# Performance work log

Hardware: AMD Instinct MI355X
Metric: run time of the kernel (lower is better)

The kernel has to match this reference:

```python
import jax, jax.numpy as jnp
import numpy as np

NEG_INF = float(np.finfo(np.float32).min)
B, QLEN, MLEN, KLEN = 2, 1024, 1024, 1024
KDIM = QDIM = ADIM = 1024
H = 16
DK = ADIM // H
SCALE = float(np.sqrt(DK))


def setup_inputs() -> dict:
    root = jax.random.key(0)
    ks = jax.random.split(root, 20)
    s = 0.02  # weight init std to keep logits well-scaled
    return {
        "key": jax.random.normal(ks[0], (B, KLEN, KDIM), jnp.float32),
        "query": jax.random.normal(ks[1], (B, QLEN, QDIM), jnp.float32),
        "memory": jax.random.normal(ks[2], (B, MLEN, KDIM), jnp.float32),
        "pos_embs": jax.random.normal(ks[3], (MLEN + KLEN, 1, QDIM), jnp.float32),
        "mask": jax.random.randint(ks[4], (B, QLEN, MLEN + KLEN), 0, 2, jnp.int32),
        "u": jax.random.normal(ks[5], (H, DK), jnp.float32) * s,
        "v": jax.random.normal(ks[6], (H, DK), jnp.float32) * s,
        "Wk": jax.random.normal(ks[7], (ADIM, KDIM), jnp.float32) * s,
        "bk": jnp.zeros((ADIM,), jnp.float32),
        "Wv": jax.random.normal(ks[8], (ADIM, KDIM), jnp.float32) * s,
        "bv": jnp.zeros((ADIM,), jnp.float32),
        "Wq": jax.random.normal(ks[9], (ADIM, QDIM), jnp.float32) * s,
        "bq": jnp.zeros((ADIM,), jnp.float32),
        "Wp": jax.random.normal(ks[10], (ADIM, QDIM), jnp.float32) * s,
        "bp": jnp.zeros((ADIM,), jnp.float32),
        "Wo": jax.random.normal(ks[11], (KDIM, ADIM), jnp.float32) * s,
        "bo": jnp.zeros((KDIM,), jnp.float32),
    }


def rel_shift(xs):
    # xs: [B, qlen, klen, H] -> TransformerXL pad/reshape shift trick
    b, q, k, h = xs.shape
    x = jnp.transpose(xs, (1, 2, 0, 3)).reshape(q, k, b * h)
    x = jnp.concatenate([jnp.zeros((q, 1, b * h), xs.dtype), x], axis=1)
    x = x.reshape(k + 1, q, b * h)[1:].reshape(q, k, b * h)
    return jnp.transpose(x.reshape(q, k, b, h), (2, 0, 1, 3))


def reference(key, query, memory, pos_embs, mask, u, v,
              Wk, bk, Wv, bv, Wq, bq, Wp, bp, Wo, bo):
    bs, qlen = query.shape[:2]
    kcat = jnp.concatenate([memory, key], axis=1)  # [B, mlen+klen, kdim]
    tk = kcat.shape[1]
    value = (kcat @ Wv.T + bv).reshape(bs, tk, H, DK)
    k = (kcat @ Wk.T + bk).reshape(bs, tk, H, DK)
    q = (query @ Wq.T + bq).reshape(bs, qlen, H, DK)
    p = (pos_embs.reshape(-1, pos_embs.shape[-1]) @ Wp.T + bp).reshape(-1, H, DK)
    AC = jnp.einsum('bihd,bjhd->bijh', q + u[None, None], k)
    BD = jnp.einsum('bihd,jhd->bijh', q + v[None, None], p)
    BD = rel_shift(BD)
    e = (AC + BD) / SCALE  # [B, qlen, mlen+klen, H]
    e = jnp.where(mask[..., None] == 0, NEG_INF, e)
    aw = jax.nn.softmax(e, axis=2)
    cv = jnp.einsum('bijh,bjhd->bihd', aw, value).reshape(bs, qlen, H * DK)
    cv = cv @ Wo.T + bo
    return cv, jnp.transpose(aw, (0, 3, 1, 2))
```

## Files before the change

kernel.cpp:

```cpp
#include <hip/hip_runtime.h>

using bf16x8 = __attribute__((ext_vector_type(8))) short;
using bf16x4 = __attribute__((ext_vector_type(4))) short;
using f32x4  = __attribute__((ext_vector_type(4))) float;

#define NH    16
#define DKH   64
#define TTOT  2048
#define QL    1024

__device__ __forceinline__ float bf2f(unsigned short u) {
  union { unsigned int i; float f; } c; c.i = ((unsigned int)u) << 16; return c.f;
}
__device__ __forceinline__ unsigned short f2bf(float f) {
  union { float f; unsigned int i; } c; c.f = f;
  unsigned int x = c.i;
  x += 0x7fffu + ((x >> 16) & 1u);
  return (unsigned short)(x >> 16);
}
__device__ __forceinline__ unsigned int cvtpk(float lo, float hi) {
  unsigned int r;
  asm("v_cvt_pk_bf16_f32 %0, %1, %2" : "=v"(r) : "v"(lo), "v"(hi));
  return r;
}
__device__ __forceinline__ int swz(int r, int c) {
  return r * 2048 + ((((c << 1) ^ ((r & 7) << 4))) >> 1);
}
__device__ __forceinline__ f32x4 mfma16(bf16x8 a, bf16x8 b, f32x4 c) {
  return __builtin_amdgcn_mfma_f32_16x16x32_bf16(a, b, c, 0, 0, 0);
}

__global__ void convert_all(
    const float* __restrict__ key, const float* __restrict__ query,
    const float* __restrict__ memory, const float* __restrict__ pos,
    const int* __restrict__ mask,
    const float* __restrict__ Wk, const float* __restrict__ Wv,
    const float* __restrict__ Wq, const float* __restrict__ Wp,
    const float* __restrict__ Wo,
    unsigned short* __restrict__ kcat, unsigned short* __restrict__ qbf,
    unsigned short* __restrict__ posb,
    unsigned short* __restrict__ wkb, unsigned short* __restrict__ wvb,
    unsigned short* __restrict__ wqb, unsigned short* __restrict__ wpb,
    unsigned short* __restrict__ wob, unsigned short* __restrict__ mkb)
{
  const int g0 = 1048576;
  const int g1 = g0 + 524288;
  const int g2 = g1 + 524288;
  const int g3 = g2 + 262144;
  const int g4 = g3 + 262144;
  const int g5 = g4 + 262144;
  const int g6 = g5 + 262144;
  const int g7 = g6 + 262144;
  const int g8 = g7 + 1048576;
  for (int g = blockIdx.x * blockDim.x + threadIdx.x; g < g8;
       g += gridDim.x * blockDim.x) {
    const float* src = nullptr;
    unsigned short* dst = nullptr;
    int i;
    if (g < g0) {
      i = g * 4;
      int b = i >> 21, r = i & ((1 << 21) - 1);
      int t = r >> 10, c = r & 1023;
      src = (t < 1024) ? memory + ((size_t)b << 20) + (t << 10) + c
                       : key + ((size_t)b << 20) + ((t - 1024) << 10) + c;
      dst = kcat + i;
    } else if (g < g1) { i = (g - g0) * 4; src = query + i; dst = qbf + i; }
    else if (g < g2)   { i = (g - g1) * 4; src = pos + i;   dst = posb + i; }
    else if (g < g3)   { i = (g - g2) * 4; src = Wk + i;    dst = wkb + i; }
    else if (g < g4)   { i = (g - g3) * 4; src = Wv + i;    dst = wvb + i; }
    else if (g < g5)   { i = (g - g4) * 4; src = Wq + i;    dst = wqb + i; }
    else if (g < g6)   { i = (g - g5) * 4; src = Wp + i;    dst = wpb + i; }
    else if (g < g7)   { i = (g - g6) * 4; src = Wo + i;    dst = wob + i; }
    else {
      i = (g - g7) * 4;
      const int4 mv = *(const int4*)(mask + i);
      const unsigned int nm = f2bf(-1e30f);
      uint2 o;
      o.x = (mv.x ? 0u : nm) | ((mv.y ? 0u : nm) << 16);
      o.y = (mv.z ? 0u : nm) | ((mv.w ? 0u : nm) << 16);
      *(uint2*)(mkb + i) = o;
      continue;
    }
    const float4 v = *(const float4*)src;
    uint2 o;
    o.x = cvtpk(v.x, v.y);
    o.y = cvtpk(v.z, v.w);
    *(uint2*)dst = o;
  }
}

#define GEMM_CORE(Aptr, Bptr) \
  f32x4 acc[4][4] = {}; \
  { \
    bf16x8 ra0 = *(const bf16x8*)Ap0; \
    bf16x8 ra1 = *(const bf16x8*)Ap1; \
    bf16x8 rb0 = *(const bf16x8*)Bp0; \
    bf16x8 rb1 = *(const bf16x8*)Bp1; \
    for (int kt = 0; kt < 32; ++kt) { \
      *(bf16x8*)(sA + swA0) = ra0; \
      *(bf16x8*)(sA + swA1) = ra1; \
      *(bf16x8*)(sB + swA0) = rb0; \
      *(bf16x8*)(sB + swA1) = rb1; \
      __syncthreads(); \
      if (kt + 1 < 32) { \
        const int o = (kt + 1) * 32; \
        ra0 = *(const bf16x8*)(Ap0 + o); \
        ra1 = *(const bf16x8*)(Ap1 + o); \
        rb0 = *(const bf16x8*)(Bp0 + o); \
        rb1 = *(const bf16x8*)(Bp1 + o); \
      } \
      bf16x8 af[4], bfr[4]; \
      _Pragma("unroll") \
      for (int mi = 0; mi < 4; ++mi) { \
        int row = wm + mi * 16 + l15; \
        af[mi] = *(const bf16x8*)(sA + row * 32 + ((l4 ^ ((row >> 1) & 3)) * 8)); \
      } \
      _Pragma("unroll") \
      for (int ni = 0; ni < 4; ++ni) { \
        int row = wn + ni * 16 + l15; \
        bfr[ni] = *(const bf16x8*)(sB + row * 32 + ((l4 ^ ((row >> 1) & 3)) * 8)); \
      } \
      _Pragma("unroll") \
      for (int mi = 0; mi < 4; ++mi) \
        _Pragma("unroll") \
        for (int ni = 0; ni < 4; ++ni) \
          acc[mi][ni] = mfma16(af[mi], bfr[ni], acc[mi][ni]); \
      __syncthreads(); \
    } \
  }

#define GEMM_PREAMBLE(Asrc, Bsrc) \
  constexpr int K = 1024; \
  __shared__ unsigned short sA[128 * 32]; \
  __shared__ unsigned short sB[128 * 32]; \
  const int tid = threadIdx.x; \
  const int lane = tid & 63; \
  const int wid = tid >> 6; \
  const int wm = (wid >> 1) * 64, wn = (wid & 1) * 64; \
  const int bm = blockIdx.y * 128, bn = blockIdx.x * 128; \
  const int l15 = lane & 15, l4 = lane >> 4; \
  const int c0 = tid, c1 = tid + 256; \
  const int am0 = c0 >> 2, as0 = c0 & 3; \
  const int am1 = c1 >> 2, as1 = c1 & 3; \
  const unsigned short* Ap0 = Asrc + (size_t)(bm + am0) * K + as0 * 8; \
  const unsigned short* Ap1 = Asrc + (size_t)(bm + am1) * K + as1 * 8; \
  const unsigned short* Bp0 = Bsrc + (size_t)(bn + am0) * K + as0 * 8; \
  const unsigned short* Bp1 = Bsrc + (size_t)(bn + am1) * K + as1 * 8; \
  const int swA0 = am0 * 32 + ((as0 ^ ((am0 >> 1) & 3)) * 8); \
  const int swA1 = am1 * 32 + ((as1 ^ ((am1 >> 1) & 3)) * 8);

__global__ __launch_bounds__(256, 2) void gemm_kv(
    const unsigned short* __restrict__ A, const unsigned short* __restrict__ Bw,
    const float* __restrict__ bk, const float* __restrict__ bv,
    unsigned short* __restrict__ kpk, unsigned short* __restrict__ vpk)
{
  GEMM_PREAMBLE(A, Bw)
  GEMM_CORE(A, Bw)
  const bool isK = bn < 1024;
  #pragma unroll
  for (int mi = 0; mi < 4; ++mi) {
    #pragma unroll
    for (int ni = 0; ni < 4; ++ni) {
      const int col = bn + wn + ni * 16 + l15;
      const int cc = col & 1023;
      const float bval = isK ? bk[cc] : bv[cc];
      #pragma unroll
      for (int j = 0; j < 4; ++j) {
        const int row = bm + wm + mi * 16 + l4 * 4 + j;
        const float cv = acc[mi][ni][j] + bval;
        const int bI = row >> 11;
        const int t = row & 2047;
        const int bh2 = bI * NH + (cc >> 6);
        if (isK) {
          const size_t o = ((((size_t)bh2 * 128 + (t >> 4)) * 8 +
                            ((cc & 63) >> 3)) * 16 + (t & 15)) * 8 + (cc & 7);
          kpk[o] = f2bf(cv);
        } else {
          const int dk = cc & 63;
          const size_t o = (((((size_t)bh2 * 4 + (dk >> 4)) * 64 + (t >> 5)) * 4 +
                            ((t >> 3) & 3)) * 16 + (dk & 15)) * 8 + (t & 7);
          vpk[o] = f2bf(cv);
        }
      }
    }
  }
}

__global__ __launch_bounds__(256, 2) void gemm_qp(
    const unsigned short* __restrict__ qry, const unsigned short* __restrict__ posb,
    const unsigned short* __restrict__ wqb, const unsigned short* __restrict__ wpb,
    const float* __restrict__ bq, const float* __restrict__ bp,
    const float* __restrict__ uvec, const float* __restrict__ vvec,
    unsigned short* __restrict__ qupk, unsigned short* __restrict__ qvpk,
    unsigned short* __restrict__ ppk)
{
  const bool isQ = blockIdx.z == 0;
  const unsigned short* A  = isQ ? qry : posb;
  const unsigned short* Bw = isQ ? wqb : wpb;
  GEMM_PREAMBLE(A, Bw)
  GEMM_CORE(A, Bw)
  #pragma unroll
  for (int mi = 0; mi < 4; ++mi) {
    #pragma unroll
    for (int ni = 0; ni < 4; ++ni) {
      const int col = bn + wn + ni * 16 + l15;
      #pragma unroll
      for (int j = 0; j < 4; ++j) {
        const int row = bm + wm + mi * 16 + l4 * 4 + j;
        if (isQ) {
          const float cv = acc[mi][ni][j] + bq[col];
          const int bI = row >> 10;
          const int t = row & 1023;
          const int bh2 = bI * NH + (col >> 6);
          const size_t o = ((((size_t)bh2 * 64 + (t >> 4)) * 8 +
                            ((col & 63) >> 3)) * 16 + (t & 15)) * 8 + (col & 7);
          qupk[o] = f2bf(cv + uvec[col]);
          qvpk[o] = f2bf(cv + vvec[col]);
        } else {
          const float cv = acc[mi][ni][j] + bp[col];
          const int t = row;
          const int h2 = col >> 6;
          const size_t o = ((((size_t)h2 * 128 + (t >> 4)) * 8 +
                            ((col & 63) >> 3)) * 16 + (t & 15)) * 8 + (col & 7);
          ppk[o] = f2bf(cv);
        }
      }
    }
  }
}

__global__ __launch_bounds__(256, 2) void gemm_out(
    const unsigned short* __restrict__ A, const unsigned short* __restrict__ Bw,
    const float* __restrict__ bias, float* __restrict__ outf)
{
  GEMM_PREAMBLE(A, Bw)
  GEMM_CORE(A, Bw)
  #pragma unroll
  for (int mi = 0; mi < 4; ++mi) {
    #pragma unroll
    for (int ni = 0; ni < 4; ++ni) {
      const int col = bn + wn + ni * 16 + l15;
      const float bval = bias[col];
      #pragma unroll
      for (int j = 0; j < 4; ++j) {
        const int row = bm + wm + mi * 16 + l4 * 4 + j;
        outf[(size_t)row * 1024 + col] = acc[mi][ni][j] + bval;
      }
    }
  }
}

__global__ __launch_bounds__(1024, 8) void attn_fused(
    const unsigned short* __restrict__ qupk, const unsigned short* __restrict__ qvpk,
    const unsigned short* __restrict__ kpk, const unsigned short* __restrict__ ppk,
    const unsigned short* __restrict__ vpk, const unsigned short* __restrict__ mkb,
    float* __restrict__ awout, unsigned short* __restrict__ cvb)
{
  __shared__ unsigned short sbd[16 * 2048];
  __shared__ float sred0[16][16];
  __shared__ float spv[3][4][16][16];
  const int tid = threadIdx.x;
  const int lane = tid & 63;
  const int w = tid >> 6;
  const int l15 = lane & 15, l4 = lane >> 4;

  const int wg = blockIdx.x;
  const int xcd = wg & 7, idx = wg >> 3;
  const int bh = xcd * 4 + (idx & 3);
  const int tI = idx >> 2;
  const int I0 = tI * 16;
  const int b = bh >> 4, h = bh & 15;

  {
    const unsigned short* qvt = qvpk + ((size_t)bh * 64 + tI) * 1024;
    bf16x8 a0 = *(const bf16x8*)(qvt + l4 * 128 + l15 * 8);
    bf16x8 a1 = *(const bf16x8*)(qvt + (4 + l4) * 128 + l15 * 8);
    const unsigned short* ppk_h = ppk + (size_t)h * 131072;
    #pragma unroll 2
    for (int nj = 0; nj < 8; ++nj) {
      const int tile = w * 8 + nj;
      const unsigned short* pt = ppk_h + (size_t)tile * 1024;
      bf16x8 b0 = *(const bf16x8*)(pt + l4 * 128 + l15 * 8);
      bf16x8 b1 = *(const bf16x8*)(pt + (4 + l4) * 128 + l15 * 8);
      f32x4 c = {0.f, 0.f, 0.f, 0.f};
      c = mfma16(a0, b0, c);
      c = mfma16(a1, b1, c);
      const int jj = tile * 16 + l15;
      #pragma unroll
      for (int j = 0; j < 4; ++j) {
        const int rl = l4 * 4 + j;
        const int r = I0 + rl;
        int dst, jp;
        if (jj >= 1023 - r) { dst = rl;     jp = jj + r - 1023; }
        else                { dst = rl - 1; jp = jj + r + 1025; }
        if (dst >= 0) sbd[swz(dst, jp)] = f2bf(c[j]);
      }
    }
    if (I0 <= 1006 && w < 8) {
      const unsigned short* qvt2 = qvpk + ((size_t)bh * 64 + tI + 1) * 1024;
      bf16x8 a0e = *(const bf16x8*)(qvt2 + l4 * 128 + l15 * 8);
      bf16x8 a1e = *(const bf16x8*)(qvt2 + (4 + l4) * 128 + l15 * 8);
      #pragma unroll 2
      for (int nj = 0; nj < 8; ++nj) {
        const int tile = w * 8 + nj;
        const unsigned short* pt = ppk_h + (size_t)tile * 1024;
        bf16x8 b0 = *(const bf16x8*)(pt + l4 * 128 + l15 * 8);
        bf16x8 b1 = *(const bf16x8*)(pt + (4 + l4) * 128 + l15 * 8);
        f32x4 c = {0.f, 0.f, 0.f, 0.f};
        c = mfma16(a0e, b0, c);
        c = mfma16(a1e, b1, c);
        const int jj = tile * 16 + l15;
        if (l4 == 0 && jj <= 1006 - I0)
          sbd[swz(15, jj + I0 + 1041)] = f2bf(c[0]);
      }
    }
    if (tid < 16) {
      const int jp = I0 + tid + 1025;
      if (jp < 2048) sbd[swz(tid, jp)] = 0;
    }
  }
  __syncthreads();

  {
    const unsigned short* qut = qupk + ((size_t)bh * 64 + tI) * 1024;
    bf16x8 a0 = *(const bf16x8*)(qut + l4 * 128 + l15 * 8);
    bf16x8 a1 = *(const bf16x8*)(qut + (4 + l4) * 128 + l15 * 8);
    const unsigned short* kpk_b = kpk + (size_t)bh * 131072;
    const unsigned short* mrow = mkb + ((size_t)b * QL + I0 + l15) * TTOT;
    const int rowbyte = l15 * 4096;
    const int sws = (l15 & 7) << 4;
    float sm = 0.f;
    #pragma unroll 2
    for (int nj = 0; nj < 8; ++nj) {
      const int tile = w * 8 + nj;
      const unsigned short* kt = kpk_b + (size_t)tile * 1024;
      bf16x8 b0 = *(const bf16x8*)(kt + l4 * 128 + l15 * 8);
      bf16x8 b1 = *(const bf16x8*)(kt + (4 + l4) * 128 + l15 * 8);
      f32x4 c = {0.f, 0.f, 0.f, 0.f};
      c = mfma16(b0, a0, c);
      c = mfma16(b1, a1, c);
      const int jp0 = tile * 16 + l4 * 4;
      char* sp = (char*)sbd + rowbyte + ((jp0 * 2) ^ sws);
      const bf16x4 bd4 = *(const bf16x4*)sp;
      const bf16x4 m4 = *(const bf16x4*)(mrow + jp0);
      bf16x4 pw;
      #pragma unroll
      for (int j = 0; j < 4; ++j) {
        const float s = (c[j] + bf2f((unsigned short)bd4[j])) * 0.125f +
                        bf2f((unsigned short)m4[j]);
        const float p = __expf(s);
        sm += p;
        pw[j] = (short)f2bf(p);
      }
      *(bf16x4*)sp = pw;
    }
    sm += __shfl_xor(sm, 16, 64);
    sm += __shfl_xor(sm, 32, 64);
    if (l4 == 0) sred0[w][l15] = sm;
  }
  __syncthreads();

  {
    const int r = w;
    float den = sred0[0][r];
    #pragma unroll
    for (int ww = 1; ww < 16; ++ww) den += sred0[ww][r];
    const float rinv = 1.0f / den;
    float* awb = awout + ((size_t)bh * QL + I0 + r) * TTOT;
    const int sws = (r & 7) << 4;
    #pragma unroll 2
    for (int q = 0; q < 4; ++q) {
      const int X = q * 1024 + lane * 16;
      bf16x8 vv = *(const bf16x8*)((const char*)sbd + r * 4096 + (X ^ sws));
      f32x4 lo, hi;
      #pragma unroll
      for (int k = 0; k < 4; ++k) {
        lo[k] = bf2f((unsigned short)vv[k]) * rinv;
        hi[k] = bf2f((unsigned short)vv[k + 4]) * rinv;
      }
      float* dp = awb + (X >> 1);
      *(f32x4*)dp = lo;
      *(f32x4*)(dp + 4) = hi;
    }
  }

  {
    const int dc = w & 3, kh = w >> 2;
    const unsigned short* vb = vpk + ((size_t)(bh * 4 + dc) * 64) * 512;
    const int sws = (l15 & 7) << 4;
    const int rowbyte = l15 * 4096;
    f32x4 pv = {0.f, 0.f, 0.f, 0.f};
    #pragma unroll 2
    for (int ks = kh * 16; ks < kh * 16 + 16; ++ks) {
      bf16x8 a = *(const bf16x8*)((const char*)sbd +
                  (rowbyte + ((ks * 64 + l4 * 16) ^ sws)));
      bf16x8 vvf = *(const bf16x8*)(vb + ks * 512 + lane * 8);
      pv = mfma16(a, vvf, pv);
    }
    if (kh) {
      #pragma unroll
      for (int j = 0; j < 4; ++j) spv[kh - 1][dc][l4 * 4 + j][l15] = pv[j];
    }
    __syncthreads();
    if (!kh) {
      const size_t obase = ((size_t)b * QL + I0 + l4 * 4) * 1024 + h * 64 + dc * 16 + l15;
      #pragma unroll
      for (int j = 0; j < 4; ++j) {
        const int rl = l4 * 4 + j;
        float den = sred0[0][rl];
        #pragma unroll
        for (int ww = 1; ww < 16; ++ww) den += sred0[ww][rl];
        const float o = (pv[j] + spv[0][dc][rl][l15] + spv[1][dc][rl][l15] +
                         spv[2][dc][rl][l15]) / den;
        cvb[obase + (size_t)j * 1024] = f2bf(o);
      }
    }
  }
}

extern "C" void kernel_launch(void* const* d_in, const int* in_sizes, int n_in,
                              void* d_out, int out_size, void* d_ws, size_t ws_size,
                              hipStream_t stream) {
  (void)in_sizes; (void)n_in; (void)out_size; (void)ws_size;
  const float* key    = (const float*)d_in[0];
  const float* query  = (const float*)d_in[1];
  const float* memory = (const float*)d_in[2];
  const float* pos    = (const float*)d_in[3];
  const int*   mask   = (const int*)d_in[4];
  const float* u      = (const float*)d_in[5];
  const float* v      = (const float*)d_in[6];
  const float* Wk     = (const float*)d_in[7];
  const float* bk     = (const float*)d_in[8];
  const float* Wv     = (const float*)d_in[9];
  const float* bv     = (const float*)d_in[10];
  const float* Wq     = (const float*)d_in[11];
  const float* bq     = (const float*)d_in[12];
  const float* Wp     = (const float*)d_in[13];
  const float* bp     = (const float*)d_in[14];
  const float* Wo     = (const float*)d_in[15];
  const float* bo     = (const float*)d_in[16];

  float* outCV = (float*)d_out;
  float* outAW = outCV + 2097152;

  char* ws = (char*)d_ws;
  const size_t MB = (size_t)1 << 20;
  unsigned short* kpk  = (unsigned short*)(ws + 0);
  unsigned short* vpk  = (unsigned short*)(ws + 8 * MB);
  unsigned short* qupk = (unsigned short*)(ws + 16 * MB);
  unsigned short* qvpk = (unsigned short*)(ws + 20 * MB);
  unsigned short* ppk  = (unsigned short*)(ws + 24 * MB);
  unsigned short* cvb  = (unsigned short*)(ws + 28 * MB);
  unsigned short* kcat = (unsigned short*)(ws + 32 * MB);
  unsigned short* qry  = (unsigned short*)(ws + 40 * MB);
  unsigned short* posb = (unsigned short*)(ws + 44 * MB);
  unsigned short* wkb  = (unsigned short*)(ws + 48 * MB);
  unsigned short* wvb  = (unsigned short*)(ws + 50 * MB);
  unsigned short* wqb  = (unsigned short*)(ws + 52 * MB);
  unsigned short* wpb  = (unsigned short*)(ws + 54 * MB);
  unsigned short* wob  = (unsigned short*)(ws + 56 * MB);
  unsigned short* mkb  = (unsigned short*)(ws + 58 * MB);

  convert_all<<<2048, 256, 0, stream>>>(key, query, memory, pos, mask,
      Wk, Wv, Wq, Wp, Wo, kcat, qry, posb, wkb, wvb, wqb, wpb, wob, mkb);

  gemm_kv<<<dim3(16, 32), 256, 0, stream>>>(kcat, wkb, bk, bv, kpk, vpk);
  gemm_qp<<<dim3(8, 16, 2), 256, 0, stream>>>(qry, posb, wqb, wpb, bq, bp,
      u, v, qupk, qvpk, ppk);

  attn_fused<<<2048, 1024, 0, stream>>>(qupk, qvpk, kpk, ppk, vpk, mkb,
      outAW, cvb);

  gemm_out<<<dim3(8, 16), 256, 0, stream>>>(cvb, wob, bo, outCV);
}
```

Baseline: 256.5 us.

## Merge projection GEMMs into one launch, truncate bf16 conversions, spread BD edge work

Combines the K/V and Q/P projection GEMMs into a single 768-block launch that picks its mode from the block index. This removes one kernel launch and lets the two groups of tiles run concurrently instead of back to back. Round-to-nearest bf16 conversion of BD values and softmax probabilities is replaced with plain truncation of the top 16 bits, which cuts ALU work but adds a small rounding bias. The extra BD row computation now uses all 16 waves with 4 tiles each instead of 8 waves with 8 tiles.

```diff
diff --git a/kernel.cpp b/kernel.cpp
--- a/kernel.cpp
+++ b/kernel.cpp
@@ -17,6 +17,9 @@
   unsigned int x = c.i;
   x += 0x7fffu + ((x >> 16) & 1u);
   return (unsigned short)(x >> 16);
+}
+__device__ __forceinline__ unsigned int fbits(float f) {
+  union { float f; unsigned int i; } c; c.f = f; return c.i;
 }
 __device__ __forceinline__ unsigned int cvtpk(float lo, float hi) {
   unsigned int r;
@@ -89,7 +92,7 @@
   }
 }
 
-#define GEMM_CORE(Aptr, Bptr) \
+#define GEMM_CORE() \
   f32x4 acc[4][4] = {}; \
   { \
     bf16x8 ra0 = *(const bf16x8*)Ap0; \
@@ -129,85 +132,72 @@
     } \
   }
 
-#define GEMM_PREAMBLE(Asrc, Bsrc) \
-  constexpr int K = 1024; \
+#define GEMM_PTRS(Asrc, Bsrc) \
+  const unsigned short* Ap0 = Asrc + (size_t)(bm + am0) * 1024 + as0 * 8; \
+  const unsigned short* Ap1 = Asrc + (size_t)(bm + am1) * 1024 + as1 * 8; \
+  const unsigned short* Bp0 = Bsrc + (size_t)(bn + am0) * 1024 + as0 * 8; \
+  const unsigned short* Bp1 = Bsrc + (size_t)(bn + am1) * 1024 + as1 * 8;
+
+#define GEMM_IDX() \
   __shared__ unsigned short sA[128 * 32]; \
   __shared__ unsigned short sB[128 * 32]; \
   const int tid = threadIdx.x; \
   const int lane = tid & 63; \
   const int wid = tid >> 6; \
   const int wm = (wid >> 1) * 64, wn = (wid & 1) * 64; \
-  const int bm = blockIdx.y * 128, bn = blockIdx.x * 128; \
   const int l15 = lane & 15, l4 = lane >> 4; \
-  const int c0 = tid, c1 = tid + 256; \
-  const int am0 = c0 >> 2, as0 = c0 & 3; \
-  const int am1 = c1 >> 2, as1 = c1 & 3; \
-  const unsigned short* Ap0 = Asrc + (size_t)(bm + am0) * K + as0 * 8; \
-  const unsigned short* Ap1 = Asrc + (size_t)(bm + am1) * K + as1 * 8; \
-  const unsigned short* Bp0 = Bsrc + (size_t)(bn + am0) * K + as0 * 8; \
-  const unsigned short* Bp1 = Bsrc + (size_t)(bn + am1) * K + as1 * 8; \
+  const int am0 = tid >> 2, as0 = tid & 3; \
+  const int am1 = (tid + 256) >> 2, as1 = (tid + 256) & 3; \
   const int swA0 = am0 * 32 + ((as0 ^ ((am0 >> 1) & 3)) * 8); \
   const int swA1 = am1 * 32 + ((as1 ^ ((am1 >> 1) & 3)) * 8);
 
-__global__ __launch_bounds__(256, 2) void gemm_kv(
-    const unsigned short* __restrict__ A, const unsigned short* __restrict__ Bw,
+__global__ __launch_bounds__(256, 2) void gemm_proj(
+    const unsigned short* __restrict__ kcat, const unsigned short* __restrict__ qry,
+    const unsigned short* __restrict__ posb,
+    const unsigned short* __restrict__ wkv, const unsigned short* __restrict__ wqb,
+    const unsigned short* __restrict__ wpb,
     const float* __restrict__ bk, const float* __restrict__ bv,
-    unsigned short* __restrict__ kpk, unsigned short* __restrict__ vpk)
+    const float* __restrict__ bq, const float* __restrict__ bp,
+    const float* __restrict__ uvec, const float* __restrict__ vvec,
+    unsigned short* __restrict__ kpk, unsigned short* __restrict__ vpk,
+    unsigned short* __restrict__ qupk, unsigned short* __restrict__ qvpk,
+    unsigned short* __restrict__ ppk)
 {
-  GEMM_PREAMBLE(A, Bw)
-  GEMM_CORE(A, Bw)
-  const bool isK = bn < 1024;
+  GEMM_IDX()
+  const int id = blockIdx.x;
+  int bm, bn, mode;
+  const unsigned short *A, *Bw;
+  if (id < 512)      { A = kcat; Bw = wkv; bm = (id >> 4) * 128; bn = (id & 15) * 128; mode = 0; }
+  else if (id < 640) { const int t = id - 512; A = qry;  Bw = wqb; bm = (t >> 3) * 128; bn = (t & 7) * 128; mode = 1; }
+  else               { const int t = id - 640; A = posb; Bw = wpb; bm = (t >> 3) * 128; bn = (t & 7) * 128; mode = 2; }
+  GEMM_PTRS(A, Bw)
+  GEMM_CORE()
   #pragma unroll
   for (int mi = 0; mi < 4; ++mi) {
     #pragma unroll
     for (int ni = 0; ni < 4; ++ni) {
       const int col = bn + wn + ni * 16 + l15;
-      const int cc = col & 1023;
-      const float bval = isK ? bk[cc] : bv[cc];
       #pragma unroll
       for (int j = 0; j < 4; ++j) {
         const int row = bm + wm + mi * 16 + l4 * 4 + j;
-        const float cv = acc[mi][ni][j] + bval;
-        const int bI = row >> 11;
-        const int t = row & 2047;
-        const int bh2 = bI * NH + (cc >> 6);
-        if (isK) {
-          const size_t o = ((((size_t)bh2 * 128 + (t >> 4)) * 8 +
-                            ((cc & 63) >> 3)) * 16 + (t & 15)) * 8 + (cc & 7);
-          kpk[o] = f2bf(cv);
-        } else {
-          const int dk = cc & 63;
-          const size_t o = (((((size_t)bh2 * 4 + (dk >> 4)) * 64 + (t >> 5)) * 4 +
-                            ((t >> 3) & 3)) * 16 + (dk & 15)) * 8 + (t & 7);
-          vpk[o] = f2bf(cv);
-        }
-      }
-    }
-  }
-}
-
-__global__ __launch_bounds__(256, 2) void gemm_qp(
-    const unsigned short* __restrict__ qry, const unsigned short* __restrict__ posb,
-    const unsigned short* __restrict__ wqb, const unsigned short* __restrict__ wpb,
-    const float* __restrict__ bq, const float* __restrict__ bp,
-    const float* __restrict__ uvec, const float* __restrict__ vvec,
-    unsigned short* __restrict__ qupk, unsigned short* __restrict__ qvpk,
-    unsigned short* __restrict__ ppk)
-{
-  const bool isQ = blockIdx.z == 0;
-  const unsigned short* A  = isQ ? qry : posb;
-  const unsigned short* Bw = isQ ? wqb : wpb;
-  GEMM_PREAMBLE(A, Bw)
-  GEMM_CORE(A, Bw)
-  #pragma unroll
-  for (int mi = 0; mi < 4; ++mi) {
-    #pragma unroll
-    for (int ni = 0; ni < 4; ++ni) {
-      const int col = bn + wn + ni * 16 + l15;
-      #pragma unroll
-      for (int j = 0; j < 4; ++j) {
-        const int row = bm + wm + mi * 16 + l4 * 4 + j;
-        if (isQ) {
+        if (mode == 0) {
+          const bool isK = col < 1024;
+          const int cc = col & 1023;
+          const float cv = acc[mi][ni][j] + (isK ? bk[cc] : bv[cc]);
+          const int bI = row >> 11;
+          const int t = row & 2047;
+          const int bh2 = bI * NH + (cc >> 6);
+          if (isK) {
+            const size_t o = ((((size_t)bh2 * 128 + (t >> 4)) * 8 +
+                              ((cc & 63) >> 3)) * 16 + (t & 15)) * 8 + (cc & 7);
+            kpk[o] = f2bf(cv);
+          } else {
+            const int dk = cc & 63;
+            const size_t o = (((((size_t)bh2 * 4 + (dk >> 4)) * 64 + (t >> 5)) * 4 +
+                              ((t >> 3) & 3)) * 16 + (dk & 15)) * 8 + (t & 7);
+            vpk[o] = f2bf(cv);
+          }
+        } else if (mode == 1) {
           const float cv = acc[mi][ni][j] + bq[col];
           const int bI = row >> 10;
           const int t = row & 1023;
@@ -233,8 +223,10 @@
     const unsigned short* __restrict__ A, const unsigned short* __restrict__ Bw,
     const float* __restrict__ bias, float* __restrict__ outf)
 {
-  GEMM_PREAMBLE(A, Bw)
-  GEMM_CORE(A, Bw)
+  GEMM_IDX()
+  const int bm = blockIdx.y * 128, bn = blockIdx.x * 128;
+  GEMM_PTRS(A, Bw)
+  GEMM_CORE()
   #pragma unroll
   for (int mi = 0; mi < 4; ++mi) {
     #pragma unroll
@@ -293,16 +285,16 @@
         int dst, jp;
         if (jj >= 1023 - r) { dst = rl;     jp = jj + r - 1023; }
         else                { dst = rl - 1; jp = jj + r + 1025; }
-        if (dst >= 0) sbd[swz(dst, jp)] = f2bf(c[j]);
-      }
-    }
-    if (I0 <= 1006 && w < 8) {
+        if (dst >= 0) sbd[swz(dst, jp)] = (unsigned short)(fbits(c[j]) >> 16);
+      }
+    }
+    if (I0 <= 1006) {
       const unsigned short* qvt2 = qvpk + ((size_t)bh * 64 + tI + 1) * 1024;
       bf16x8 a0e = *(const bf16x8*)(qvt2 + l4 * 128 + l15 * 8);
       bf16x8 a1e = *(const bf16x8*)(qvt2 + (4 + l4) * 128 + l15 * 8);
       #pragma unroll 2
-      for (int nj = 0; nj < 8; ++nj) {
-        const int tile = w * 8 + nj;
+      for (int nj = 0; nj < 4; ++nj) {
+        const int tile = w * 4 + nj;
         const unsigned short* pt = ppk_h + (size_t)tile * 1024;
         bf16x8 b0 = *(const bf16x8*)(pt + l4 * 128 + l15 * 8);
         bf16x8 b1 = *(const bf16x8*)(pt + (4 + l4) * 128 + l15 * 8);
@@ -311,7 +303,7 @@
         c = mfma16(a1e, b1, c);
         const int jj = tile * 16 + l15;
         if (l4 == 0 && jj <= 1006 - I0)
-          sbd[swz(15, jj + I0 + 1041)] = f2bf(c[0]);
+          sbd[swz(15, jj + I0 + 1041)] = (unsigned short)(fbits(c[0]) >> 16);
       }
     }
     if (tid < 16) {
@@ -343,16 +335,18 @@
       char* sp = (char*)sbd + rowbyte + ((jp0 * 2) ^ sws);
       const bf16x4 bd4 = *(const bf16x4*)sp;
       const bf16x4 m4 = *(const bf16x4*)(mrow + jp0);
-      bf16x4 pw;
+      float p[4];
       #pragma unroll
       for (int j = 0; j < 4; ++j) {
         const float s = (c[j] + bf2f((unsigned short)bd4[j])) * 0.125f +
                         bf2f((unsigned short)m4[j]);
-        const float p = __expf(s);
-        sm += p;
-        pw[j] = (short)f2bf(p);
-      }
-      *(bf16x4*)sp = pw;
+        p[j] = __expf(s);
+        sm += p[j];
+      }
+      uint2 pw;
+      pw.x = (fbits(p[1]) & 0xffff0000u) | (fbits(p[0]) >> 16);
+      pw.y = (fbits(p[3]) & 0xffff0000u) | (fbits(p[2]) >> 16);
+      *(uint2*)sp = pw;
     }
     sm += __shfl_xor(sm, 16, 64);
     sm += __shfl_xor(sm, 32, 64);
@@ -464,9 +458,8 @@
   convert_all<<<2048, 256, 0, stream>>>(key, query, memory, pos, mask,
       Wk, Wv, Wq, Wp, Wo, kcat, qry, posb, wkb, wvb, wqb, wpb, wob, mkb);
 
-  gemm_kv<<<dim3(16, 32), 256, 0, stream>>>(kcat, wkb, bk, bv, kpk, vpk);
-  gemm_qp<<<dim3(8, 16, 2), 256, 0, stream>>>(qry, posb, wqb, wpb, bq, bp,
-      u, v, qupk, qvpk, ppk);
+  gemm_proj<<<768, 256, 0, stream>>>(kcat, qry, posb, wkb, wqb, wpb,
+      bk, bv, bq, bp, u, v, kpk, vpk, qupk, qvpk, ppk);
 
   attn_fused<<<2048, 1024, 0, stream>>>(qupk, qvpk, kpk, ppk, vpk, mkb,
       outAW, cvb);
```

After: 241.9 us. -5.7%, faster.
